# Performance work log

Hardware: AMD Instinct MI355X
Metric: run time of the kernel (lower is better)

## Reference

```python
import jax, jax.numpy as jnp
import numpy as np

EPS = 1e-6
NUM_HEADS = 4
GSIZE = (2, 2, 2)


def _ln_channels_first(x, w, b):
    # LayerNorm over channel dim (axis=1) of [B,C,D,H,W]
    u = x.mean(1, keepdims=True)
    s = ((x - u) ** 2).mean(1, keepdims=True)
    xn = (x - u) / jnp.sqrt(s + EPS)
    return w[None, :, None, None, None] * xn + b[None, :, None, None, None]


def setup_inputs() -> dict:
    key = jax.random.key(0)
    ks = jax.random.split(key, 7)
    B, C = 2, 256
    x2 = jax.random.normal(ks[0], (B, C, 32, 32, 32), jnp.float32)
    x1_low = jax.random.normal(ks[1], (B, C, 16, 16, 16), jnp.float32)
    sc = 1.0 / np.sqrt(C).astype(np.float32)
    q_w = jax.random.normal(ks[2], (C, C), jnp.float32) * sc
    k_w = jax.random.normal(ks[3], (C, C), jnp.float32) * sc
    v_w = jax.random.normal(ks[4], (C, C), jnp.float32) * sc
    dw_w = jax.random.normal(ks[5], (C, 1, 3, 3, 3), jnp.float32) * (1.0 / np.sqrt(27.0).astype(np.float32))
    proj_w = jax.random.normal(ks[6], (C, C), jnp.float32) * sc
    nq_w = jnp.ones((C,), jnp.float32)
    nq_b = jnp.zeros((C,), jnp.float32)
    nkv_w = jnp.ones((C,), jnp.float32)
    nkv_b = jnp.zeros((C,), jnp.float32)
    return {"x2": x2, "x1_low": x1_low, "q_w": q_w, "k_w": k_w, "v_w": v_w,
            "dw_w": dw_w, "proj_w": proj_w, "nq_w": nq_w, "nq_b": nq_b,
            "nkv_w": nkv_w, "nkv_b": nkv_b}


def reference(x2, x1_low, q_w, k_w, v_w, dw_w, proj_w, nq_w, nq_b, nkv_w, nkv_b):
    B, C, D, H, W = x2.shape
    h = NUM_HEADS
    d = C // h
    gD, gH, gW = GSIZE
    _, _, Dl, Hl, Wl = x1_low.shape

    # adaptive_avg_pool3d to (gD,gH,gW): dims divisible -> block means
    tokens = x1_low.reshape(B, C, gD, Dl // gD, gH, Hl // gH, gW, Wl // gW).mean((3, 5, 7))
    # depthwise 3x3x3 conv, padding 1
    dw = jax.lax.conv_general_dilated(
        tokens, dw_w, window_strides=(1, 1, 1), padding='SAME',
        dimension_numbers=('NCDHW', 'OIDHW', 'NCDHW'), feature_group_count=C)
    tokens = tokens + dw

    N = D * H * W
    g = gD * gH * gW

    qx = _ln_channels_first(x2, nq_w, nq_b).reshape(B, C, N)
    q = jnp.einsum('oc,bcn->bon', q_w, qx).reshape(B, h, d, N).transpose(0, 1, 3, 2)  # [B,h,N,d]

    tk = _ln_channels_first(tokens, nkv_w, nkv_b).reshape(B, C, g)
    k = jnp.einsum('oc,bcg->bog', k_w, tk).reshape(B, h, d, g)  # [B,h,d,g]
    v = jnp.einsum('oc,bcg->bog', v_w, tokens.reshape(B, C, g)).reshape(B, h, d, g).transpose(0, 1, 3, 2)  # [B,h,g,d]

    attn = jax.nn.softmax(jnp.einsum('bhnd,bhdg->bhng', q, k) / jnp.sqrt(jnp.float32(d)), axis=-1)
    out = jnp.einsum('bhng,bhgd->bhnd', attn, v)  # [B,h,N,d]
    out = out.transpose(0, 1, 3, 2).reshape(B, C, N)
    return jnp.einsum('oc,bcn->bon', proj_w, out).reshape(B, C, D, H, W)
```

## Files before the change

kernel.cpp:

```cpp
#include <hip/hip_runtime.h>
#include <math.h>

#define EPS 1e-6f

typedef __attribute__((ext_vector_type(8))) short bhalf8;
typedef __attribute__((ext_vector_type(4))) float floatx4;

__device__ __forceinline__ unsigned short f2bf(float f) {
    union { float f; unsigned u; } v; v.f = f;
    unsigned r = (v.u + 0x7fffu + ((v.u >> 16) & 1u)) >> 16;
    return (unsigned short)r;
}
__device__ __forceinline__ float bflo(unsigned u) {
    union { unsigned x; float f; } v; v.x = u << 16; return v.f;
}
__device__ __forceinline__ float bfhi(unsigned u) {
    union { unsigned x; float f; } v; v.x = u & 0xffff0000u; return v.f;
}

__global__ void pre1(const float* __restrict__ q_w,
                     const float* __restrict__ proj_w,
                     const float* __restrict__ nq_w,
                     const float* __restrict__ nq_b,
                     unsigned short* __restrict__ W1b,
                     unsigned short* __restrict__ W2b,
                     float* __restrict__ A, float* __restrict__ Bc,
                     const float* __restrict__ x1, float* __restrict__ tokens) {
    if (blockIdx.x < 256) {
        int o = blockIdx.x;
        int c = threadIdx.x;
        float qv = q_w[o * 256 + c];
        float pv = proj_w[o * 256 + c];
        float w1 = qv * nq_w[c];
        int kc = c >> 5, kk = c & 31;
        W1b[kc * 8192 + o * 32 + kk] = f2bf(w1);
        W2b[kc * 8192 + o * 32 + kk] = f2bf(pv);
        float bcv = qv * nq_b[c];
        __shared__ float sA[4], sB[4];
        float a = w1, b = bcv;
        for (int off = 32; off > 0; off >>= 1) {
            a += __shfl_down(a, off);
            b += __shfl_down(b, off);
        }
        int wave = threadIdx.x >> 6, lane = threadIdx.x & 63;
        if (lane == 0) { sA[wave] = a; sB[wave] = b; }
        __syncthreads();
        if (threadIdx.x == 0) {
            A[o]  = sA[0] + sA[1] + sA[2] + sA[3];
            Bc[o] = sB[0] + sB[1] + sB[2] + sB[3];
        }
    } else {
        int bc = blockIdx.x - 256;
        const float* base = x1 + (size_t)bc * 4096;
        int wave = threadIdx.x >> 6;
        int lane = threadIdx.x & 63;
        int doff = lane >> 3, hoff = lane & 7;
        for (int t = wave * 2; t < wave * 2 + 2; ++t) {
            int gd = t >> 2, gh = (t >> 1) & 1, gw = t & 1;
            const float* p = base + (gd * 8 + doff) * 256 + (gh * 8 + hoff) * 16 + gw * 8;
            float4 v0 = *(const float4*)p;
            float4 v1 = *(const float4*)(p + 4);
            float s = v0.x + v0.y + v0.z + v0.w + v1.x + v1.y + v1.z + v1.w;
            for (int off = 32; off > 0; off >>= 1) s += __shfl_down(s, off);
            if (lane == 0) tokens[bc * 8 + t] = s * (1.0f / 512.0f);
        }
    }
}

__global__ void tokens_all(const float* __restrict__ tokens,
                           const float* __restrict__ dw_w,
                           const float* __restrict__ nkv_w,
                           const float* __restrict__ nkv_b,
                           const float* __restrict__ k_w,
                           const float* __restrict__ v_w,
                           unsigned short* __restrict__ kkb,
                           float* __restrict__ vv) {
    int b = blockIdx.x >> 6;
    int og = blockIdx.x & 63;
    int c = threadIdx.x;
    __shared__ float t2[256][9];
    __shared__ float u8[8], r8[8];
    float t[8];
    #pragma unroll
    for (int g = 0; g < 8; ++g) t[g] = tokens[(b * 256 + c) * 8 + g];
    float w[27];
    #pragma unroll
    for (int i = 0; i < 27; ++i) w[i] = dw_w[c * 27 + i];
    #pragma unroll
    for (int z = 0; z < 2; ++z)
    #pragma unroll
    for (int y = 0; y < 2; ++y)
    #pragma unroll
    for (int x = 0; x < 2; ++x) {
        float s = 0.f;
        #pragma unroll
        for (int i = 0; i < 3; ++i) {
            int nz = z + i - 1; if (nz < 0 || nz > 1) continue;
            #pragma unroll
            for (int j = 0; j < 3; ++j) {
                int ny = y + j - 1; if (ny < 0 || ny > 1) continue;
                #pragma unroll
                for (int l = 0; l < 3; ++l) {
                    int nx = x + l - 1; if (nx < 0 || nx > 1) continue;
                    s += w[(i * 3 + j) * 3 + l] * t[nz * 4 + ny * 2 + nx];
                }
            }
        }
        int g = z * 4 + y * 2 + x;
        t2[c][g] = t[g] + s;
    }
    __syncthreads();
    if (c < 8) {
        float su = 0.f, sq = 0.f;
        for (int cc = 0; cc < 256; ++cc) { float v = t2[cc][c]; su += v; sq += v * v; }
        float u = su * (1.f / 256.f);
        float var = sq * (1.f / 256.f) - u * u;
        u8[c] = u;
        r8[c] = rsqrtf(var + EPS);
    }
    __syncthreads();
    int wv = threadIdx.x >> 6;
    int lane = threadIdx.x & 63;
    int o = og * 4 + wv;
    float acck[8] = {0,0,0,0,0,0,0,0}, accv[8] = {0,0,0,0,0,0,0,0};
    #pragma unroll
    for (int i = 0; i < 4; ++i) {
        int cc = lane + 64 * i;
        float kw = k_w[o * 256 + cc];
        float vw = v_w[o * 256 + cc];
        float nw = nkv_w[cc], nb2 = nkv_b[cc];
        #pragma unroll
        for (int g = 0; g < 8; ++g) {
            float tv = t2[cc][g];
            acck[g] += kw * (nw * (tv - u8[g]) * r8[g] + nb2);
            accv[g] += vw * tv;
        }
    }
    #pragma unroll
    for (int g = 0; g < 8; ++g)
        for (int off = 32; off > 0; off >>= 1) {
            acck[g] += __shfl_down(acck[g], off);
            accv[g] += __shfl_down(accv[g], off);
        }
    if (lane == 0) {
        #pragma unroll
        for (int g = 0; g < 8; ++g) {
            kkb[b * 2048 + o * 8 + g] = f2bf(acck[g]);
            vv[b * 2048 + (o >> 6) * 512 + g * 64 + (o & 63)] = accv[g];
        }
    }
}

__global__ __launch_bounds__(512, 4)
void fused2(const float* __restrict__ x2,
            const unsigned short* __restrict__ W1b,
            const unsigned short* __restrict__ W2b,
            const float* __restrict__ Ag, const float* __restrict__ Bg,
            const unsigned short* __restrict__ kkb,
            const float* __restrict__ vvf,
            float* __restrict__ out) {
    __shared__ __align__(16) unsigned short XQ[16384];
    __shared__ __align__(16) float KVP[3072];
    __shared__ __align__(16) float part[1024];
    __shared__ __align__(16) float As[256], Bs[256];
    __shared__ float us[64], rs[64];

    const int tid = threadIdx.x;
    const int w = tid >> 6;
    const int lane = tid & 63;
    const int m = lane & 15;
    const int qd = lane >> 4;
    const int n0g = blockIdx.x * 64;
    const int b = n0g >> 15;
    const int pos0 = n0g & 32767;

    uint4 kreg;
    if (tid < 256) kreg = ((const uint4*)(kkb + b * 2048))[tid];
    float4 vreg = ((const float4*)(vvf + b * 2048))[tid];
    if (tid < 256) { As[tid] = Ag[tid]; Bs[tid] = Bg[tid]; }
    const unsigned short* w1p = W1b + (size_t)(32 * w + m) * 32 + qd * 8;
    bhalf8 af1_0 = *(const bhalf8*)(w1p);
    bhalf8 af1_1 = *(const bhalf8*)(w1p + 512);

    {
        const int n4 = tid & 15, cg = tid >> 4;
        const float* xb = x2 + (size_t)b * 8388608 + pos0 + n4 * 4;
        float su[4] = {0,0,0,0}, sq[4] = {0,0,0,0};
        #pragma unroll
        for (int cc = 0; cc < 4; ++cc) {
            int p = cg + 32 * cc;
            int c0 = 2 * p;
            float4 a  = *(const float4*)(xb + (size_t)c0 * 32768);
            float4 bq = *(const float4*)(xb + (size_t)(c0 + 1) * 32768);
            int g = p >> 2, wsub = p & 3;
            float av[4] = {a.x, a.y, a.z, a.w};
            float bv[4] = {bq.x, bq.y, bq.z, bq.w};
            #pragma unroll
            for (int i = 0; i < 4; ++i) {
                su[i] += av[i] + bv[i];
                sq[i] += av[i] * av[i] + bv[i] * bv[i];
                int row = 4 * n4 + i;
                int swz = ((row >> 2) ^ row) & 7;
                unsigned val = (unsigned)f2bf(av[i]) | ((unsigned)f2bf(bv[i]) << 16);
                ((unsigned*)XQ)[row * 128 + ((g ^ swz) << 2) + wsub] = val;
            }
        }
        if (tid < 256) ((uint4*)KVP)[tid] = kreg;
        ((float4*)(KVP + 1024))[tid] = vreg;
        #pragma unroll
        for (int i = 0; i < 4; ++i) {
            float a2 = su[i], q2 = sq[i];
            a2 += __shfl_down(a2, 16); q2 += __shfl_down(q2, 16);
            a2 += __shfl_down(a2, 32); q2 += __shfl_down(q2, 32);
            if (lane < 16) {
                part[w * 128 + (4 * lane + i) * 2]     = a2;
                part[w * 128 + (4 * lane + i) * 2 + 1] = q2;
            }
        }
    }
    __syncthreads();

    if (tid < 64) {
        float S = 0.f, Q = 0.f;
        #pragma unroll
        for (int w8 = 0; w8 < 8; ++w8) {
            S += part[w8 * 128 + tid * 2];
            Q += part[w8 * 128 + tid * 2 + 1];
        }
        float mu = S * (1.f / 256.f);
        us[tid] = mu;
        rs[tid] = rsqrtf(Q * (1.f / 256.f) - mu * mu + EPS);
    }

    floatx4 acc[2][4];
    #pragma unroll
    for (int i = 0; i < 2; ++i)
        #pragma unroll
        for (int j = 0; j < 4; ++j)
            acc[i][j] = (floatx4){0.f, 0.f, 0.f, 0.f};
    {
        bhalf8 afb[2][2];
        afb[0][0] = af1_0; afb[0][1] = af1_1;
        #pragma unroll
        for (int kc = 0; kc < 8; ++kc) {
            if (kc < 7) {
                afb[(kc + 1) & 1][0] = *(const bhalf8*)(w1p + (kc + 1) * 8192);
                afb[(kc + 1) & 1][1] = *(const bhalf8*)(w1p + (kc + 1) * 8192 + 512);
            }
            bhalf8 bfr[4];
            #pragma unroll
            for (int nt = 0; nt < 4; ++nt) {
                int n = nt * 16 + m;
                int swz = ((n >> 2) ^ n) & 7;
                bfr[nt] = *(const bhalf8*)(XQ + n * 256 + (((4 * kc + qd) ^ swz) << 3));
            }
            #pragma unroll
            for (int t = 0; t < 2; ++t)
                #pragma unroll
                for (int nt = 0; nt < 4; ++nt)
                    acc[t][nt] = __builtin_amdgcn_mfma_f32_16x16x32_bf16(afb[kc & 1][t], bfr[nt], acc[t][nt], 0, 0, 0);
        }
    }
    const unsigned short* w2p = W2b + (size_t)(32 * w + m) * 32 + qd * 8;
    bhalf8 af2_0 = *(const bhalf8*)(w2p);
    bhalf8 af2_1 = *(const bhalf8*)(w2p + 512);
    __syncthreads();

    #pragma unroll
    for (int t = 0; t < 2; ++t) {
        int ob = 32 * w + 16 * t + 4 * qd;
        floatx4 Af = *(const floatx4*)&As[ob];
        floatx4 Bf = *(const floatx4*)&Bs[ob];
        int gq = ob >> 3, off = ob & 7;
        #pragma unroll
        for (int nt = 0; nt < 4; ++nt) {
            int n = nt * 16 + m;
            int swz = ((n >> 2) ^ n) & 7;
            float uv = us[n], rv = rs[n];
            unsigned p0 = (unsigned)f2bf(rv * (acc[t][nt][0] - uv * Af[0]) + Bf[0])
                        | ((unsigned)f2bf(rv * (acc[t][nt][1] - uv * Af[1]) + Bf[1]) << 16);
            unsigned p1 = (unsigned)f2bf(rv * (acc[t][nt][2] - uv * Af[2]) + Bf[2])
                        | ((unsigned)f2bf(rv * (acc[t][nt][3] - uv * Af[3]) + Bf[3]) << 16);
            uint2 val; val.x = p0; val.y = p1;
            *(uint2*)(XQ + n * 256 + ((gq ^ swz) << 3) + off) = val;
        }
    }
    __syncthreads();

    {
        const int h = w & 3;
        const int an = ((w >> 2) << 5) | (lane & 31);
        const int dh = lane >> 5;
        const int sw = ((an >> 2) ^ an) & 7;
        unsigned short* qrow = XQ + an * 256;
        uint4 q4[4];
        #pragma unroll
        for (int gl = 0; gl < 4; ++gl)
            q4[gl] = *(const uint4*)(qrow + (((8 * h + 4 * dh + gl) ^ sw) << 3));
        float lg[8] = {0, 0, 0, 0, 0, 0, 0, 0};
        const unsigned short* kh = (const unsigned short*)KVP + h * 512 + dh * 256;
        #pragma unroll
        for (int dp = 0; dp < 16; ++dp) {
            unsigned qq = ((const unsigned*)q4)[dp];
            float q0 = bflo(qq), q1 = bfhi(qq);
            uint4 k0 = *(const uint4*)(kh + dp * 16);
            uint4 k1 = *(const uint4*)(kh + dp * 16 + 8);
            lg[0] += q0 * bflo(k0.x); lg[1] += q0 * bfhi(k0.x);
            lg[2] += q0 * bflo(k0.y); lg[3] += q0 * bfhi(k0.y);
            lg[4] += q0 * bflo(k0.z); lg[5] += q0 * bfhi(k0.z);
            lg[6] += q0 * bflo(k0.w); lg[7] += q0 * bfhi(k0.w);
            lg[0] += q1 * bflo(k1.x); lg[1] += q1 * bfhi(k1.x);
            lg[2] += q1 * bflo(k1.y); lg[3] += q1 * bfhi(k1.y);
            lg[4] += q1 * bflo(k1.z); lg[5] += q1 * bfhi(k1.z);
            lg[6] += q1 * bflo(k1.w); lg[7] += q1 * bfhi(k1.w);
        }
        #pragma unroll
        for (int g = 0; g < 8; ++g) lg[g] += __shfl_xor(lg[g], 32);
        float mx = lg[0];
        #pragma unroll
        for (int g = 1; g < 8; ++g) mx = fmaxf(mx, lg[g]);
        float p[8], s = 0.f;
        #pragma unroll
        for (int g = 0; g < 8; ++g) { p[g] = __expf((lg[g] - mx) * 0.125f); s += p[g]; }
        float is = 1.f / s;
        #pragma unroll
        for (int g = 0; g < 8; ++g) p[g] *= is;
        float o2[32];
        #pragma unroll
        for (int j = 0; j < 32; ++j) o2[j] = 0.f;
        const float* vh = KVP + 1024 + h * 512 + dh * 32;
        #pragma unroll
        for (int g = 0; g < 8; ++g) {
            float pg = p[g];
            #pragma unroll
            for (int j = 0; j < 8; ++j) {
                float4 v4 = *(const float4*)(vh + g * 64 + j * 4);
                o2[4 * j + 0] += pg * v4.x;
                o2[4 * j + 1] += pg * v4.y;
                o2[4 * j + 2] += pg * v4.z;
                o2[4 * j + 3] += pg * v4.w;
            }
        }
        #pragma unroll
        for (int gl = 0; gl < 4; ++gl) {
            uint4 pk;
            pk.x = (unsigned)f2bf(o2[8 * gl + 0]) | ((unsigned)f2bf(o2[8 * gl + 1]) << 16);
            pk.y = (unsigned)f2bf(o2[8 * gl + 2]) | ((unsigned)f2bf(o2[8 * gl + 3]) << 16);
            pk.z = (unsigned)f2bf(o2[8 * gl + 4]) | ((unsigned)f2bf(o2[8 * gl + 5]) << 16);
            pk.w = (unsigned)f2bf(o2[8 * gl + 6]) | ((unsigned)f2bf(o2[8 * gl + 7]) << 16);
            *(uint4*)(qrow + (((8 * h + 4 * dh + gl) ^ sw) << 3)) = pk;
        }
    }
    __syncthreads();

    floatx4 acc2[2][4];
    #pragma unroll
    for (int i = 0; i < 2; ++i)
        #pragma unroll
        for (int j = 0; j < 4; ++j)
            acc2[i][j] = (floatx4){0.f, 0.f, 0.f, 0.f};
    {
        bhalf8 afb[2][2];
        afb[0][0] = af2_0; afb[0][1] = af2_1;
        #pragma unroll
        for (int kc = 0; kc < 8; ++kc) {
            if (kc < 7) {
                afb[(kc + 1) & 1][0] = *(const bhalf8*)(w2p + (kc + 1) * 8192);
                afb[(kc + 1) & 1][1] = *(const bhalf8*)(w2p + (kc + 1) * 8192 + 512);
            }
            bhalf8 bfr[4];
            #pragma unroll
            for (int nt = 0; nt < 4; ++nt) {
                int n = nt * 16 + m;
                int swz = ((n >> 2) ^ n) & 7;
                bfr[nt] = *(const bhalf8*)(XQ + n * 256 + (((4 * kc + qd) ^ swz) << 3));
            }
            #pragma unroll
            for (int t = 0; t < 2; ++t)
                #pragma unroll
                for (int nt = 0; nt < 4; ++nt)
                    acc2[t][nt] = __builtin_amdgcn_mfma_f32_16x16x32_bf16(afb[kc & 1][t], bfr[nt], acc2[t][nt], 0, 0, 0);
        }
    }

    {
        float* tb = KVP + w * 320;
        float* obase = out + (size_t)b * 8388608 + pos0;
        const int ol = lane >> 2, c4 = lane & 3;
        #pragma unroll
        for (int t = 0; t < 2; ++t) {
            #pragma unroll
            for (int nt = 0; nt < 4; ++nt) {
                #pragma unroll
                for (int rr = 0; rr < 4; ++rr)
                    tb[(qd * 4 + rr) * 20 + m] = acc2[t][nt][rr];
                float4 vo = *(const float4*)(tb + ol * 20 + c4 * 4);
                *(float4*)(obase + (size_t)(32 * w + 16 * t + ol) * 32768 + nt * 16 + c4 * 4) = vo;
            }
        }
    }
}

extern "C" void kernel_launch(void* const* d_in, const int* in_sizes, int n_in,
                              void* d_out, int out_size, void* d_ws, size_t ws_size,
                              hipStream_t stream) {
    (void)in_sizes; (void)n_in; (void)out_size; (void)ws_size;
    const float* x2     = (const float*)d_in[0];
    const float* x1_low = (const float*)d_in[1];
    const float* q_w    = (const float*)d_in[2];
    const float* k_w    = (const float*)d_in[3];
    const float* v_w    = (const float*)d_in[4];
    const float* dw_w   = (const float*)d_in[5];
    const float* proj_w = (const float*)d_in[6];
    const float* nq_w   = (const float*)d_in[7];
    const float* nq_b   = (const float*)d_in[8];
    const float* nkv_w  = (const float*)d_in[9];
    const float* nkv_b  = (const float*)d_in[10];
    float* outp = (float*)d_out;

    float* wsf = (float*)d_ws;
    float* Av  = wsf;
    float* Bv  = wsf + 256;
    float* tk  = wsf + 512;
    float* vvf = wsf + 4608;
    unsigned short* kkb = (unsigned short*)(wsf + 8704);
    unsigned short* W1b = (unsigned short*)(wsf + 10752);
    unsigned short* W2b = (unsigned short*)(wsf + 43520);

    pre1<<<768, 256, 0, stream>>>(q_w, proj_w, nq_w, nq_b, W1b, W2b, Av, Bv, x1_low, tk);
    tokens_all<<<128, 256, 0, stream>>>(tk, dw_w, nkv_w, nkv_b, k_w, v_w, kkb, vvf);
    fused2<<<1024, 512, 0, stream>>>(x2, W1b, W2b, Av, Bv, kkb, vvf, outp);
}
```

Baseline: 174.7 us.

## Compute attention logits and PV with MFMA using pre-packed K/V fragments

Replaces the scalar per-token attention (QK dot products and softmax-weighted V accumulation from LDS) with bf16 MFMA instructions. The tokens kernel now writes K and V directly in MFMA fragment layout (zero-padded, V in bf16), so fused2 loads them straight into registers and no longer stages them in shared memory. This shrinks LDS and raises the launch-bounds occupancy hint from 4 to 8. It also swizzles the output transpose buffer to avoid bank conflicts. V is now rounded to bf16, and the padded MFMA wastes part of each instruction.

```diff
diff --git a/kernel.cpp b/kernel.cpp
--- a/kernel.cpp
+++ b/kernel.cpp
@@ -10,12 +10,6 @@
     union { float f; unsigned u; } v; v.f = f;
     unsigned r = (v.u + 0x7fffu + ((v.u >> 16) & 1u)) >> 16;
     return (unsigned short)r;
-}
-__device__ __forceinline__ float bflo(unsigned u) {
-    union { unsigned x; float f; } v; v.x = u << 16; return v.f;
-}
-__device__ __forceinline__ float bfhi(unsigned u) {
-    union { unsigned x; float f; } v; v.x = u & 0xffff0000u; return v.f;
 }
 
 __global__ void pre1(const float* __restrict__ q_w,
@@ -73,8 +67,8 @@
                            const float* __restrict__ nkv_b,
                            const float* __restrict__ k_w,
                            const float* __restrict__ v_w,
-                           unsigned short* __restrict__ kkb,
-                           float* __restrict__ vv) {
+                           unsigned short* __restrict__ kfragG,
+                           unsigned short* __restrict__ vfragG) {
     int b = blockIdx.x >> 6;
     int og = blockIdx.x & 63;
     int c = threadIdx.x;
@@ -143,27 +137,39 @@
             accv[g] += __shfl_down(accv[g], off);
         }
     if (lane == 0) {
+        int h = o >> 6, dl = o & 63;
+        int kc = dl >> 5, dd = (dl >> 3) & 3, j = dl & 7;
+        unsigned short* kb = kfragG + (size_t)(((b * 4 + h) * 2 + kc) * 512) + j;
         #pragma unroll
         for (int g = 0; g < 8; ++g) {
-            kkb[b * 2048 + o * 8 + g] = f2bf(acck[g]);
-            vv[b * 2048 + (o >> 6) * 512 + g * 64 + (o & 63)] = accv[g];
-        }
+            kb[(g + 16 * dd) * 8] = f2bf(acck[g]);
+            kb[(g + 8 + 16 * dd) * 8] = 0;
+        }
+        int dt = dl >> 4, l15 = dl & 15;
+        uint4 pk;
+        pk.x = (unsigned)f2bf(accv[0]) | ((unsigned)f2bf(accv[1]) << 16);
+        pk.y = (unsigned)f2bf(accv[2]) | ((unsigned)f2bf(accv[3]) << 16);
+        pk.z = (unsigned)f2bf(accv[4]) | ((unsigned)f2bf(accv[5]) << 16);
+        pk.w = (unsigned)f2bf(accv[6]) | ((unsigned)f2bf(accv[7]) << 16);
+        *(uint4*)(vfragG + (size_t)(((b * 4 + h) * 4 + dt) * 128) + l15 * 8) = pk;
     }
 }
 
-__global__ __launch_bounds__(512, 4)
+__global__ __launch_bounds__(512, 8)
 void fused2(const float* __restrict__ x2,
             const unsigned short* __restrict__ W1b,
             const unsigned short* __restrict__ W2b,
             const float* __restrict__ Ag, const float* __restrict__ Bg,
-            const unsigned short* __restrict__ kkb,
-            const float* __restrict__ vvf,
+            const unsigned short* __restrict__ kfragG,
+            const unsigned short* __restrict__ vfragG,
             float* __restrict__ out) {
     __shared__ __align__(16) unsigned short XQ[16384];
-    __shared__ __align__(16) float KVP[3072];
-    __shared__ __align__(16) float part[1024];
-    __shared__ __align__(16) float As[256], Bs[256];
-    __shared__ float us[64], rs[64];
+    __shared__ __align__(16) float SCR[2048];
+    float* part = SCR;
+    float* As   = SCR + 1024;
+    float* Bs   = SCR + 1280;
+    float* us   = SCR + 1536;
+    float* rs   = SCR + 1600;
 
     const int tid = threadIdx.x;
     const int w = tid >> 6;
@@ -174,9 +180,6 @@
     const int b = n0g >> 15;
     const int pos0 = n0g & 32767;
 
-    uint4 kreg;
-    if (tid < 256) kreg = ((const uint4*)(kkb + b * 2048))[tid];
-    float4 vreg = ((const float4*)(vvf + b * 2048))[tid];
     if (tid < 256) { As[tid] = Ag[tid]; Bs[tid] = Bg[tid]; }
     const unsigned short* w1p = W1b + (size_t)(32 * w + m) * 32 + qd * 8;
     bhalf8 af1_0 = *(const bhalf8*)(w1p);
@@ -205,8 +208,6 @@
                 ((unsigned*)XQ)[row * 128 + ((g ^ swz) << 2) + wsub] = val;
             }
         }
-        if (tid < 256) ((uint4*)KVP)[tid] = kreg;
-        ((float4*)(KVP + 1024))[tid] = vreg;
         #pragma unroll
         for (int i = 0; i < 4; ++i) {
             float a2 = su[i], q2 = sq[i];
@@ -289,66 +290,56 @@
 
     {
         const int h = w & 3;
-        const int an = ((w >> 2) << 5) | (lane & 31);
-        const int dh = lane >> 5;
-        const int sw = ((an >> 2) ^ an) & 7;
-        unsigned short* qrow = XQ + an * 256;
-        uint4 q4[4];
-        #pragma unroll
-        for (int gl = 0; gl < 4; ++gl)
-            q4[gl] = *(const uint4*)(qrow + (((8 * h + 4 * dh + gl) ^ sw) << 3));
-        float lg[8] = {0, 0, 0, 0, 0, 0, 0, 0};
-        const unsigned short* kh = (const unsigned short*)KVP + h * 512 + dh * 256;
-        #pragma unroll
-        for (int dp = 0; dp < 16; ++dp) {
-            unsigned qq = ((const unsigned*)q4)[dp];
-            float q0 = bflo(qq), q1 = bfhi(qq);
-            uint4 k0 = *(const uint4*)(kh + dp * 16);
-            uint4 k1 = *(const uint4*)(kh + dp * 16 + 8);
-            lg[0] += q0 * bflo(k0.x); lg[1] += q0 * bfhi(k0.x);
-            lg[2] += q0 * bflo(k0.y); lg[3] += q0 * bfhi(k0.y);
-            lg[4] += q0 * bflo(k0.z); lg[5] += q0 * bfhi(k0.z);
-            lg[6] += q0 * bflo(k0.w); lg[7] += q0 * bfhi(k0.w);
-            lg[0] += q1 * bflo(k1.x); lg[1] += q1 * bfhi(k1.x);
-            lg[2] += q1 * bflo(k1.y); lg[3] += q1 * bfhi(k1.y);
-            lg[4] += q1 * bflo(k1.z); lg[5] += q1 * bfhi(k1.z);
-            lg[6] += q1 * bflo(k1.w); lg[7] += q1 * bfhi(k1.w);
-        }
-        #pragma unroll
-        for (int g = 0; g < 8; ++g) lg[g] += __shfl_xor(lg[g], 32);
-        float mx = lg[0];
-        #pragma unroll
-        for (int g = 1; g < 8; ++g) mx = fmaxf(mx, lg[g]);
-        float p[8], s = 0.f;
-        #pragma unroll
-        for (int g = 0; g < 8; ++g) { p[g] = __expf((lg[g] - mx) * 0.125f); s += p[g]; }
-        float is = 1.f / s;
-        #pragma unroll
-        for (int g = 0; g < 8; ++g) p[g] *= is;
-        float o2[32];
-        #pragma unroll
-        for (int j = 0; j < 32; ++j) o2[j] = 0.f;
-        const float* vh = KVP + 1024 + h * 512 + dh * 32;
-        #pragma unroll
-        for (int g = 0; g < 8; ++g) {
-            float pg = p[g];
-            #pragma unroll
-            for (int j = 0; j < 8; ++j) {
-                float4 v4 = *(const float4*)(vh + g * 64 + j * 4);
-                o2[4 * j + 0] += pg * v4.x;
-                o2[4 * j + 1] += pg * v4.y;
-                o2[4 * j + 2] += pg * v4.z;
-                o2[4 * j + 3] += pg * v4.w;
-            }
-        }
-        #pragma unroll
-        for (int gl = 0; gl < 4; ++gl) {
-            uint4 pk;
-            pk.x = (unsigned)f2bf(o2[8 * gl + 0]) | ((unsigned)f2bf(o2[8 * gl + 1]) << 16);
-            pk.y = (unsigned)f2bf(o2[8 * gl + 2]) | ((unsigned)f2bf(o2[8 * gl + 3]) << 16);
-            pk.z = (unsigned)f2bf(o2[8 * gl + 4]) | ((unsigned)f2bf(o2[8 * gl + 5]) << 16);
-            pk.w = (unsigned)f2bf(o2[8 * gl + 6]) | ((unsigned)f2bf(o2[8 * gl + 7]) << 16);
-            *(uint4*)(qrow + (((8 * h + 4 * dh + gl) ^ sw) << 3)) = pk;
+        const int nh = w >> 2;
+        uint4 kf0 = ((const uint4*)(kfragG + (size_t)((b * 4 + h) * 2 + 0) * 512))[lane];
+        uint4 kf1 = ((const uint4*)(kfragG + (size_t)((b * 4 + h) * 2 + 1) * 512))[lane];
+        uint4 vf[4];
+        #pragma unroll
+        for (int dt = 0; dt < 4; ++dt) {
+            uint4 z; z.x = 0; z.y = 0; z.z = 0; z.w = 0;
+            if (lane < 16) z = ((const uint4*)(vfragG + (size_t)((b * 4 + h) * 4 + dt) * 128))[lane];
+            vf[dt] = z;
+        }
+        #pragma unroll
+        for (int nt2 = 0; nt2 < 2; ++nt2) {
+            const int n = (2 * nh + nt2) * 16 + m;
+            const int swz = ((n >> 2) ^ n) & 7;
+            unsigned short* qrow = XQ + n * 256;
+            floatx4 s4 = (floatx4){0.f, 0.f, 0.f, 0.f};
+            bhalf8 qf0 = *(const bhalf8*)(qrow + (((h * 8 + qd) ^ swz) << 3));
+            bhalf8 qf1 = *(const bhalf8*)(qrow + (((h * 8 + 4 + qd) ^ swz) << 3));
+            s4 = __builtin_amdgcn_mfma_f32_16x16x32_bf16(*(const bhalf8*)&kf0, qf0, s4, 0, 0, 0);
+            s4 = __builtin_amdgcn_mfma_f32_16x16x32_bf16(*(const bhalf8*)&kf1, qf1, s4, 0, 0, 0);
+            float sv0 = s4[0] * 0.125f, sv1 = s4[1] * 0.125f;
+            float sv2 = s4[2] * 0.125f, sv3 = s4[3] * 0.125f;
+            float m4 = fmaxf(fmaxf(sv0, sv1), fmaxf(sv2, sv3));
+            float mm = fmaxf(m4, __shfl_xor(m4, 16));
+            float p0 = __expf(sv0 - mm), p1 = __expf(sv1 - mm);
+            float p2 = __expf(sv2 - mm), p3 = __expf(sv3 - mm);
+            float ss = p0 + p1 + p2 + p3;
+            float inv = 1.f / (ss + __shfl_xor(ss, 16));
+            p0 *= inv; p1 *= inv; p2 *= inv; p3 *= inv;
+            float e0 = __shfl_xor(p0, 16), e1 = __shfl_xor(p1, 16);
+            float e2 = __shfl_xor(p2, 16), e3 = __shfl_xor(p3, 16);
+            uint4 pbu; pbu.x = 0; pbu.y = 0; pbu.z = 0; pbu.w = 0;
+            if (qd == 0) {
+                pbu.x = (unsigned)f2bf(p0) | ((unsigned)f2bf(p1) << 16);
+                pbu.y = (unsigned)f2bf(p2) | ((unsigned)f2bf(p3) << 16);
+                pbu.z = (unsigned)f2bf(e0) | ((unsigned)f2bf(e1) << 16);
+                pbu.w = (unsigned)f2bf(e2) | ((unsigned)f2bf(e3) << 16);
+            }
+            bhalf8 pb = *(const bhalf8*)&pbu;
+            #pragma unroll
+            for (int dt = 0; dt < 4; ++dt) {
+                floatx4 o4 = (floatx4){0.f, 0.f, 0.f, 0.f};
+                o4 = __builtin_amdgcn_mfma_f32_16x16x32_bf16(*(const bhalf8*)&vf[dt], pb, o4, 0, 0, 0);
+                int cb = h * 64 + dt * 16 + 4 * qd;
+                int gl = cb >> 3;
+                uint2 w2v;
+                w2v.x = (unsigned)f2bf(o4[0]) | ((unsigned)f2bf(o4[1]) << 16);
+                w2v.y = (unsigned)f2bf(o4[2]) | ((unsigned)f2bf(o4[3]) << 16);
+                *(uint2*)(qrow + ((gl ^ swz) << 3) + (cb & 7)) = w2v;
+            }
         }
     }
     __syncthreads();
@@ -384,7 +375,7 @@
     }
 
     {
-        float* tb = KVP + w * 320;
+        float* tb = SCR + w * 256;
         float* obase = out + (size_t)b * 8388608 + pos0;
         const int ol = lane >> 2, c4 = lane & 3;
         #pragma unroll
@@ -392,9 +383,11 @@
             #pragma unroll
             for (int nt = 0; nt < 4; ++nt) {
                 #pragma unroll
-                for (int rr = 0; rr < 4; ++rr)
-                    tb[(qd * 4 + rr) * 20 + m] = acc2[t][nt][rr];
-                float4 vo = *(const float4*)(tb + ol * 20 + c4 * 4);
+                for (int rr = 0; rr < 4; ++rr) {
+                    int row = qd * 4 + rr;
+                    tb[row * 16 + (m ^ (row & 12))] = acc2[t][nt][rr];
+                }
+                float4 vo = *(const float4*)(tb + ol * 16 + ((c4 * 4) ^ (ol & 12)));
                 *(float4*)(obase + (size_t)(32 * w + 16 * t + ol) * 32768 + nt * 16 + c4 * 4) = vo;
             }
         }
@@ -422,12 +415,12 @@
     float* Av  = wsf;
     float* Bv  = wsf + 256;
     float* tk  = wsf + 512;
-    float* vvf = wsf + 4608;
-    unsigned short* kkb = (unsigned short*)(wsf + 8704);
+    unsigned short* kfragG = (unsigned short*)(wsf + 4608);
+    unsigned short* vfragG = (unsigned short*)(wsf + 8704);
     unsigned short* W1b = (unsigned short*)(wsf + 10752);
     unsigned short* W2b = (unsigned short*)(wsf + 43520);
 
     pre1<<<768, 256, 0, stream>>>(q_w, proj_w, nq_w, nq_b, W1b, W2b, Av, Bv, x1_low, tk);
-    tokens_all<<<128, 256, 0, stream>>>(tk, dw_w, nkv_w, nkv_b, k_w, v_w, kkb, vvf);
-    fused2<<<1024, 512, 0, stream>>>(x2, W1b, W2b, Av, Bv, kkb, vvf, outp);
+    tokens_all<<<128, 256, 0, stream>>>(tk, dw_w, nkv_w, nkv_b, k_w, v_w, kfragG, vfragG);
+    fused2<<<1024, 512, 0, stream>>>(x2, W1b, W2b, Av, Bv, kfragG, vfragG, outp);
 }
```

Result: slower. 341.8 us (+95.6%).
